# Performance work log

Measured on AMD Instinct MI355X. Metric: run time of the kernel, lower is better.

## Reference

```python
import jax, jax.numpy as jnp
import numpy as np

B, N, H, D, K, HEADS = 128, 64, 256, 128, 8, 3


def _ln(x, g, b):
    mu = x.mean(-1, keepdims=True)
    var = x.var(-1, keepdims=True)
    return (x - mu) * jax.lax.rsqrt(var + 1e-5) * g + b


def _mmlp2(x, W1, b1, g1, be1, W2, b2):
    # per-node batched MLP: [B,N,in] x [N,in,out] -> [B,N,out]
    h = jnp.einsum('bni,nio->bno', x, W1) + b1
    h = jax.nn.relu(_ln(h, g1, be1))
    return jnp.einsum('bni,nio->bno', h, W2) + b2


def _chi(x, m1, m2):
    # 2-additive Mobius Choquet integral, averaged over heads.
    # x: [B,S,K,D], m1: [S,heads,K] (singleton Mobius), m2: [S,heads,K,K] (pair Mobius, upper-tri)
    tri = jnp.triu(jnp.ones((K, K), x.dtype), k=1)
    pairmin = jnp.minimum(x[:, :, :, None, :], x[:, :, None, :, :])  # [B,S,K,K,D]
    single = jnp.einsum('shk,bskd->bsd', m1, x)
    pair = jnp.einsum('shij,bsijd->bsd', m2 * tri, pairmin)
    return (single + pair) / HEADS


def setup_inputs() -> dict:
    key = jax.random.key(0)
    ks = jax.random.split(key, 10)
    s = lambda k, *sh: (jax.random.normal(k, sh, jnp.float32) * 0.05)
    inp = {}
    inp['observation'] = jax.random.normal(ks[0], (B, N, H), jnp.float32)
    inp['action'] = jax.random.normal(ks[1], (B, N, H), jnp.float32)
    inp['local_edges'] = jax.random.randint(ks[2], (N, 2, K + 1), 0, N)
    inp['V_W1'] = s(ks[3], N, H, H);   inp['V_b1'] = jnp.zeros((N, H), jnp.float32)
    inp['V_g1'] = jnp.ones((H,), jnp.float32); inp['V_beta1'] = jnp.zeros((H,), jnp.float32)
    inp['V_W2'] = s(ks[4], N, H, D);   inp['V_b2'] = jnp.zeros((N, D), jnp.float32)
    inp['A_W1'] = s(ks[5], N, 2 * H, H); inp['A_b1'] = jnp.zeros((N, H), jnp.float32)
    inp['A_g1'] = jnp.ones((H,), jnp.float32); inp['A_beta1'] = jnp.zeros((H,), jnp.float32)
    inp['A_W2'] = s(ks[6], N, H, D);   inp['A_b2'] = jnp.zeros((N, D), jnp.float32)
    inp['chi_m1'] = s(ks[7], N, HEADS, K)
    inp['chi_m2'] = s(ks[8], N, HEADS, K, K)
    return inp


def reference(observation, action, local_edges, V_W1, V_b1, V_g1, V_beta1, V_W2, V_b2,
              A_W1, A_b1, A_g1, A_beta1, A_W2, A_b2, chi_m1, chi_m2):
    V = _mmlp2(observation, V_W1, V_b1, V_g1, V_beta1, V_W2, V_b2)          # [B,N,D]
    A = _mmlp2(jnp.concatenate([observation, action], -1),
               A_W1, A_b1, A_g1, A_beta1, A_W2, A_b2)                       # [B,N,D]
    Q = A + V
    centers = local_edges[:, 0, 0]   # [S]
    neigh = local_edges[:, 0, 1:]    # [S,K]
    # .data in torch detaches the gathered neighbors
    Qn = jax.lax.stop_gradient(Q[:, neigh, :])   # [B,S,K,D]
    Vn = jax.lax.stop_gradient(V[:, neigh, :])
    chi_q = (_chi(Qn, chi_m1, chi_m2) + Q[:, centers, :]).mean(-1)  # [B,S]
    chi_v = (_chi(Vn, chi_m1, chi_m2) + V[:, centers, :]).mean(-1)  # [B,S]
    return chi_q, chi_v
```

## Files before the change

### kernel.cpp

```cpp
#include <hip/hip_runtime.h>
#include <hip/hip_bf16.h>

#define BCNT 128
#define NNODE 64
#define HDIM 256
#define DDIM 128
#define KNEI 8
#define NR (BCNT * NNODE)

typedef __attribute__((ext_vector_type(8))) short bf16x8;
typedef __attribute__((ext_vector_type(8))) unsigned short ushort8;
typedef __attribute__((ext_vector_type(16))) float f32x16;

__device__ __forceinline__ unsigned short f2bf(float f) {
    union { __hip_bfloat16 b; unsigned short u; } c;
    c.b = __float2bfloat16(f);
    return c.u;
}
__device__ __forceinline__ float bf2f(unsigned short u) {
    union { unsigned short u; __hip_bfloat16 b; } c;
    c.u = u;
    return __bfloat162float(c.b);
}

__global__ __launch_bounds__(256) void xsplit(
    const float* __restrict__ obs, const float* __restrict__ act,
    ushort* __restrict__ obsH, ushort* __restrict__ obsL,
    ushort* __restrict__ actH, ushort* __restrict__ actL)
{
    size_t i = ((size_t)blockIdx.x * 256 + threadIdx.x) * 4;
    const size_t NT = (size_t)NR * HDIM;
    const float* src; ushort *dh, *dl;
    if (i < NT) { src = obs; dh = obsH; dl = obsL; }
    else        { i -= NT; src = act; dh = actH; dl = actL; }
    float4 v = *(const float4*)(src + i);
    ushort4 h4, l4;
    h4.x = f2bf(v.x); l4.x = f2bf(v.x - bf2f(h4.x));
    h4.y = f2bf(v.y); l4.y = f2bf(v.y - bf2f(h4.y));
    h4.z = f2bf(v.z); l4.z = f2bf(v.z - bf2f(h4.z));
    h4.w = f2bf(v.w); l4.w = f2bf(v.w - bf2f(h4.w));
    *(ushort4*)(dh + i) = h4;
    *(ushort4*)(dl + i) = l4;
}

template<int KDIM>
__global__ __launch_bounds__(128) void mlp1_mfma(
    const ushort* __restrict__ obsH, const ushort* __restrict__ obsL,
    const ushort* __restrict__ actH, const ushort* __restrict__ actL,
    const float* __restrict__ W1, const float* __restrict__ b1,
    float* __restrict__ h, float* __restrict__ statsP)
{
    const int id = blockIdx.x;
    const int s_ = (id >> 3) & 3;
    const int g_ = ((id >> 5) << 3) | (id & 7);
    const int n  = g_ >> 2;
    const int cb = g_ & 3;
    const int bm = s_ * 32;

    const int tid = threadIdx.x;
    const int l = tid & 63;
    const int wc = tid >> 6;
    const int lo32 = l & 31, gg = l >> 5;

    __shared__ __align__(16) ushort xs[2][2][32 * 40];
    __shared__ float sstat[2][32][2];

    const int oW = cb * 64 + wc * 32 + lo32;
    const float* wp = W1 + (size_t)n * KDIM * HDIM + oW;

    const int sm = tid >> 2, sc = tid & 3;
    const size_t xrow = ((size_t)(bm + sm) * NNODE + n) * HDIM;

    f32x16 acc = {};
    ushort8 xh, xl;
    float wvA_[16], wvB_[16];

    auto loadX = [&](int k0) {
        const ushort *sh = obsH, *sl = obsL;
        int kk = k0;
        if (KDIM == 512 && k0 >= 256) { sh = actH; sl = actL; kk = k0 - 256; }
        xh = *(const ushort8*)(sh + xrow + kk + sc * 8);
        xl = *(const ushort8*)(sl + xrow + kk + sc * 8);
    };

#define LOADW1(k0, wv) { _Pragma("unroll") for (int kb = 0; kb < 2; ++kb) { _Pragma("unroll") for (int i = 0; i < 8; ++i) wv[kb*8+i] = wp[(size_t)((k0) + kb*16 + gg*8 + i) * HDIM]; } }

#define STEP1(k0, buf, wvC, wvN) { \
    *(ushort8*)&xs[buf][0][sm * 40 + sc * 8] = xh; \
    *(ushort8*)&xs[buf][1][sm * 40 + sc * 8] = xl; \
    __syncthreads(); \
    if ((k0) + 32 < KDIM) { loadX((k0) + 32); LOADW1((k0) + 32, wvN); } \
    _Pragma("unroll") for (int kb = 0; kb < 2; ++kb) { \
        bf16x8 ahi = *(const bf16x8*)&xs[buf][0][lo32 * 40 + kb * 16 + gg * 8]; \
        bf16x8 alo = *(const bf16x8*)&xs[buf][1][lo32 * 40 + kb * 16 + gg * 8]; \
        bf16x8 bhi, blo; \
        _Pragma("unroll") for (int i = 0; i < 8; ++i) { \
            float f = wvC[kb*8+i]; \
            unsigned short hh = f2bf(f); \
            bhi[i] = (short)hh; \
            blo[i] = (short)f2bf(f - bf2f(hh)); \
        } \
        acc = __builtin_amdgcn_mfma_f32_32x32x16_bf16(ahi, bhi, acc, 0, 0, 0); \
        acc = __builtin_amdgcn_mfma_f32_32x32x16_bf16(ahi, blo, acc, 0, 0, 0); \
        acc = __builtin_amdgcn_mfma_f32_32x32x16_bf16(alo, bhi, acc, 0, 0, 0); \
    } \
}

    loadX(0);
    LOADW1(0, wvA_);
    #pragma unroll
    for (int k0 = 0; k0 < KDIM; k0 += 64) {
        STEP1(k0, 0, wvA_, wvB_);
        STEP1(k0 + 32, 1, wvB_, wvA_);
    }
#undef STEP1
#undef LOADW1

    float bias = b1[(size_t)n * HDIM + oW];
    #pragma unroll
    for (int r = 0; r < 16; ++r) {
        int mm = (r & 3) + 8 * (r >> 2) + 4 * gg;
        float v = acc[r] + bias;
        h[((size_t)(bm + mm) * NNODE + n) * HDIM + oW] = v;
        float a = v, q = v * v;
        #pragma unroll
        for (int off = 16; off >= 1; off >>= 1) {
            a += __shfl_xor(a, off);
            q += __shfl_xor(q, off);
        }
        if (lo32 == 0) { sstat[wc][mm][0] = a; sstat[wc][mm][1] = q; }
    }
    __syncthreads();
    if (tid < 32) {
        float s1 = sstat[0][tid][0] + sstat[1][tid][0];
        float s2 = sstat[0][tid][1] + sstat[1][tid][1];
        size_t row = (size_t)(bm + tid) * NNODE + n;
        statsP[((size_t)cb * NR + row) * 2 + 0] = s1;
        statsP[((size_t)cb * NR + row) * 2 + 1] = s2;
    }
}

__global__ __launch_bounds__(256) void lnsplit(
    const float* __restrict__ hV, const float* __restrict__ hA,
    const float* __restrict__ stV, const float* __restrict__ stA,
    const float* __restrict__ Vg1, const float* __restrict__ Vbe1,
    const float* __restrict__ Ag1, const float* __restrict__ Abe1,
    ushort* __restrict__ hbVH, ushort* __restrict__ hbVL,
    ushort* __restrict__ hbAH, ushort* __restrict__ hbAL)
{
    const int br = blockIdx.y;
    const float* hp = br ? hA : hV;
    const float* st = br ? stA : stV;
    const float* gp = br ? Ag1 : Vg1;
    const float* bp = br ? Abe1 : Vbe1;
    ushort* oh = br ? hbAH : hbVH;
    ushort* ol = br ? hbAL : hbVL;

    const int tid = threadIdx.x;
    const int row = blockIdx.x * 4 + (tid >> 6);
    const int c4 = (tid & 63) * 4;

    float s1 = 0.f, s2 = 0.f;
    #pragma unroll
    for (int cb = 0; cb < 4; ++cb) {
        s1 += st[((size_t)cb * NR + row) * 2 + 0];
        s2 += st[((size_t)cb * NR + row) * 2 + 1];
    }
    float mu = s1 * (1.0f / 256.0f);
    float rs = rsqrtf(s2 * (1.0f / 256.0f) - mu * mu + 1e-5f);

    float4 v = *(const float4*)(hp + (size_t)row * HDIM + c4);
    float4 gv = *(const float4*)(gp + c4);
    float4 bv = *(const float4*)(bp + c4);
    float y0 = fmaxf((v.x - mu) * rs * gv.x + bv.x, 0.0f);
    float y1 = fmaxf((v.y - mu) * rs * gv.y + bv.y, 0.0f);
    float y2 = fmaxf((v.z - mu) * rs * gv.z + bv.z, 0.0f);
    float y3 = fmaxf((v.w - mu) * rs * gv.w + bv.w, 0.0f);
    ushort4 h4, l4;
    h4.x = f2bf(y0); l4.x = f2bf(y0 - bf2f(h4.x));
    h4.y = f2bf(y1); l4.y = f2bf(y1 - bf2f(h4.y));
    h4.z = f2bf(y2); l4.z = f2bf(y2 - bf2f(h4.z));
    h4.w = f2bf(y3); l4.w = f2bf(y3 - bf2f(h4.w));
    *(ushort4*)(oh + (size_t)row * HDIM + c4) = h4;
    *(ushort4*)(ol + (size_t)row * HDIM + c4) = l4;
}

__global__ __launch_bounds__(128) void mlp2_mfma(
    const ushort* __restrict__ hbVH, const ushort* __restrict__ hbVL,
    const ushort* __restrict__ hbAH, const ushort* __restrict__ hbAL,
    const float* __restrict__ VW2, const float* __restrict__ Vb2,
    const float* __restrict__ AW2, const float* __restrict__ Ab2,
    float* __restrict__ Vout, float* __restrict__ Aout)
{
    const int id = blockIdx.x;
    const int s_ = (id >> 3) & 3;
    const int g_ = ((id >> 5) << 3) | (id & 7);
    const int n  = g_ >> 2;
    const int cb = g_ & 1;
    const int br = (g_ >> 1) & 1;
    const int bm = s_ * 32;

    const int tid = threadIdx.x;
    const int l = tid & 63;
    const int wc = tid >> 6;
    const int lo32 = l & 31, gg = l >> 5;

    __shared__ __align__(16) ushort xs[2][2][32 * 40];

    const int oW = cb * 64 + wc * 32 + lo32;
    const float* wp = (br ? AW2 : VW2) + (size_t)n * HDIM * DDIM + oW;
    const ushort* xph = br ? hbAH : hbVH;
    const ushort* xpl = br ? hbAL : hbVL;

    const int sm = tid >> 2, sc = tid & 3;
    const size_t xrow = ((size_t)(bm + sm) * NNODE + n) * HDIM;

    f32x16 acc = {};
    ushort8 xh, xl;
    float wvA_[16], wvB_[16];

    auto loadX = [&](int k0) {
        xh = *(const ushort8*)(xph + xrow + k0 + sc * 8);
        xl = *(const ushort8*)(xpl + xrow + k0 + sc * 8);
    };

#define LOADW2(k0, wv) { _Pragma("unroll") for (int kb = 0; kb < 2; ++kb) { _Pragma("unroll") for (int i = 0; i < 8; ++i) wv[kb*8+i] = wp[(size_t)((k0) + kb*16 + gg*8 + i) * DDIM]; } }

#define STEP2(k0, buf, wvC, wvN) { \
    *(ushort8*)&xs[buf][0][sm * 40 + sc * 8] = xh; \
    *(ushort8*)&xs[buf][1][sm * 40 + sc * 8] = xl; \
    __syncthreads(); \
    if ((k0) + 32 < HDIM) { loadX((k0) + 32); LOADW2((k0) + 32, wvN); } \
    _Pragma("unroll") for (int kb = 0; kb < 2; ++kb) { \
        bf16x8 ahi = *(const bf16x8*)&xs[buf][0][lo32 * 40 + kb * 16 + gg * 8]; \
        bf16x8 alo = *(const bf16x8*)&xs[buf][1][lo32 * 40 + kb * 16 + gg * 8]; \
        bf16x8 bhi, blo; \
        _Pragma("unroll") for (int i = 0; i < 8; ++i) { \
            float f = wvC[kb*8+i]; \
            unsigned short hh = f2bf(f); \
            bhi[i] = (short)hh; \
            blo[i] = (short)f2bf(f - bf2f(hh)); \
        } \
        acc = __builtin_amdgcn_mfma_f32_32x32x16_bf16(ahi, bhi, acc, 0, 0, 0); \
        acc = __builtin_amdgcn_mfma_f32_32x32x16_bf16(ahi, blo, acc, 0, 0, 0); \
        acc = __builtin_amdgcn_mfma_f32_32x32x16_bf16(alo, bhi, acc, 0, 0, 0); \
    } \
}

    loadX(0);
    LOADW2(0, wvA_);
    #pragma unroll
    for (int k0 = 0; k0 < HDIM; k0 += 64) {
        STEP2(k0, 0, wvA_, wvB_);
        STEP2(k0 + 32, 1, wvB_, wvA_);
    }
#undef STEP2
#undef LOADW2

    float bias = (br ? Ab2 : Vb2)[(size_t)n * DDIM + oW];
    float* outp = br ? Aout : Vout;
    #pragma unroll
    for (int r = 0; r < 16; ++r) {
        int mm = (r & 3) + 8 * (r >> 2) + 4 * gg;
        outp[((size_t)(bm + mm) * NNODE + n) * DDIM + oW] = acc[r] + bias;
    }
}

__global__ __launch_bounds__(128) void chi_kernel(
    const float* __restrict__ V, const float* __restrict__ A,
    const int* __restrict__ le, const float* __restrict__ m1,
    const float* __restrict__ m2, float* __restrict__ out)
{
    const int n = blockIdx.x;
    const int b = blockIdx.y;
    const int tid = threadIdx.x;

    __shared__ float sm1[KNEI];
    __shared__ float sm2[KNEI * KNEI];
    __shared__ int   sidx[KNEI + 1];
    __shared__ float pq[2], pv[2];

    if (tid < KNEI) {
        float s = 0.0f;
        #pragma unroll
        for (int hh = 0; hh < 3; ++hh) s += m1[n * 24 + hh * 8 + tid];
        sm1[tid] = s;
    }
    if (tid < 64) {
        int i = tid >> 3, j = tid & 7;
        float s = 0.0f;
        if (j > i) {
            #pragma unroll
            for (int hh = 0; hh < 3; ++hh) s += m2[n * 192 + hh * 64 + tid];
        }
        sm2[tid] = s;
    }
    if (tid < KNEI + 1) sidx[tid] = le[n * 18 + tid];
    __syncthreads();

    const float* Vb_ = V + (size_t)b * (NNODE * DDIM);
    const float* Ab_ = A + (size_t)b * (NNODE * DDIM);
    const int cen = sidx[0];

    float vn[KNEI], qn[KNEI];
    #pragma unroll
    for (int k = 0; k < KNEI; ++k) {
        int nb = sidx[1 + k];
        float vv = Vb_[nb * DDIM + tid];
        float aa = Ab_[nb * DDIM + tid];
        vn[k] = vv;
        qn[k] = vv + aa;
    }

    float sq = 0.0f, sv = 0.0f;
    #pragma unroll
    for (int k = 0; k < KNEI; ++k) { sq += sm1[k] * qn[k]; sv += sm1[k] * vn[k]; }
    #pragma unroll
    for (int i = 0; i < KNEI; ++i) {
        #pragma unroll
        for (int j = i + 1; j < KNEI; ++j) {
            float w = sm2[i * 8 + j];
            sq += w * fminf(qn[i], qn[j]);
            sv += w * fminf(vn[i], vn[j]);
        }
    }

    float Vc = Vb_[cen * DDIM + tid];
    float Ac = Ab_[cen * DDIM + tid];
    float valq = sq * (1.0f / 3.0f) + (Vc + Ac);
    float valv = sv * (1.0f / 3.0f) + Vc;

    #pragma unroll
    for (int o = 32; o; o >>= 1) {
        valq += __shfl_down(valq, o);
        valv += __shfl_down(valv, o);
    }
    if ((tid & 63) == 0) { pq[tid >> 6] = valq; pv[tid >> 6] = valv; }
    __syncthreads();
    if (tid == 0) {
        out[b * NNODE + n]                = (pq[0] + pq[1]) * (1.0f / 128.0f);
        out[BCNT * NNODE + b * NNODE + n] = (pv[0] + pv[1]) * (1.0f / 128.0f);
    }
}

extern "C" void kernel_launch(void* const* d_in, const int* in_sizes, int n_in,
                              void* d_out, int out_size, void* d_ws, size_t ws_size,
                              hipStream_t stream)
{
    const float* obs  = (const float*)d_in[0];
    const float* act  = (const float*)d_in[1];
    const int*   le   = (const int*)  d_in[2];
    const float* VW1  = (const float*)d_in[3];
    const float* Vb1  = (const float*)d_in[4];
    const float* Vg1  = (const float*)d_in[5];
    const float* Vbe1 = (const float*)d_in[6];
    const float* VW2  = (const float*)d_in[7];
    const float* Vb2  = (const float*)d_in[8];
    const float* AW1  = (const float*)d_in[9];
    const float* Ab1  = (const float*)d_in[10];
    const float* Ag1  = (const float*)d_in[11];
    const float* Abe1 = (const float*)d_in[12];
    const float* AW2  = (const float*)d_in[13];
    const float* Ab2  = (const float*)d_in[14];
    const float* m1   = (const float*)d_in[15];
    const float* m2   = (const float*)d_in[16];
    float* out = (float*)d_out;

    float* hV  = (float*)d_ws;
    float* hA  = hV + (size_t)NR * HDIM;
    float* V   = hA + (size_t)NR * HDIM;
    float* A   = V  + (size_t)NR * DDIM;
    float* stV = A  + (size_t)NR * DDIM;
    float* stA = stV + (size_t)4 * NR * 2;
    ushort* up = (ushort*)(stA + (size_t)4 * NR * 2);
    const size_t P = (size_t)NR * HDIM;
    ushort* obsH = up;          ushort* obsL = obsH + P;
    ushort* actH = obsL + P;    ushort* actL = actH + P;
    ushort* hbVH = actL + P;    ushort* hbVL = hbVH + P;
    ushort* hbAH = hbVL + P;    ushort* hbAL = hbAH + P;

    xsplit<<<dim3(4096), dim3(256), 0, stream>>>(obs, act, obsH, obsL, actH, actL);
    mlp1_mfma<256><<<dim3(1024), dim3(128), 0, stream>>>(obsH, obsL, actH, actL,
                                                         VW1, Vb1, hV, stV);
    mlp1_mfma<512><<<dim3(1024), dim3(128), 0, stream>>>(obsH, obsL, actH, actL,
                                                         AW1, Ab1, hA, stA);
    lnsplit<<<dim3(NR / 4, 2), dim3(256), 0, stream>>>(hV, hA, stV, stA,
                                                       Vg1, Vbe1, Ag1, Abe1,
                                                       hbVH, hbVL, hbAH, hbAL);
    mlp2_mfma<<<dim3(1024), dim3(128), 0, stream>>>(hbVH, hbVL, hbAH, hbAL,
                                                    VW2, Vb2, AW2, Ab2, V, A);
    chi_kernel<<<dim3(NNODE, BCNT), dim3(128), 0, stream>>>(V, A, le, m1, m2, out);
}
```

Before: 203.1 us.

## Pre-split and transpose weights, fuse MLP layer-1 with LayerNorm epilogue

Adds a wsplit kernel that transposes all four weight tensors and splits them once into bf16 hi/lo planes. The MFMA kernels can then load B fragments as contiguous 16-byte vectors instead of strided scalar fp32 loads with per-element conversion. The V and A layer-1 GEMMs merge into one 256-thread kernel where each block covers the full 256-wide hidden row. That lets LayerNorm statistics, ReLU and the hi/lo split run in the epilogue, which removes the fp32 hidden buffer, the partial-stats buffer and the separate lnsplit pass. In exchange the weights are re-split on every call, adding one extra pass over them, and mlp1 now runs fewer, larger blocks that hold more registers.

```diff
diff --git a/kernel.cpp b/kernel.cpp
--- a/kernel.cpp
+++ b/kernel.cpp
@@ -8,6 +8,12 @@
 #define KNEI 8
 #define NR (BCNT * NNODE)
 
+#define OFF1V 0
+#define OFF1A 4194304
+#define OFF2V 12582912
+#define OFF2A 14680064
+#define WTOT  16777216
+
 typedef __attribute__((ext_vector_type(8))) short bf16x8;
 typedef __attribute__((ext_vector_type(8))) unsigned short ushort8;
 typedef __attribute__((ext_vector_type(16))) float f32x16;
@@ -21,6 +27,50 @@
     union { unsigned short u; __hip_bfloat16 b; } c;
     c.u = u;
     return __bfloat162float(c.b);
+}
+__device__ __forceinline__ void split2(float f, unsigned short& h, unsigned short& l) {
+    h = f2bf(f);
+    l = f2bf(f - bf2f(h));
+}
+
+__global__ __launch_bounds__(256) void wsplit(
+    const float* __restrict__ VW1, const float* __restrict__ AW1,
+    const float* __restrict__ VW2, const float* __restrict__ AW2,
+    ushort* __restrict__ WtH, ushort* __restrict__ WtL)
+{
+    const int n = blockIdx.y;
+    const int t = blockIdx.x;
+    const float* src; size_t dbase; int K, OUT, tk, to;
+    if (t < 16)      { src = VW1 + (size_t)n*65536;  dbase = OFF1V + (size_t)n*65536;  K=256; OUT=256; tk=t>>2;      to=t&3;      }
+    else if (t < 48) { src = AW1 + (size_t)n*131072; dbase = OFF1A + (size_t)n*131072; K=512; OUT=256; tk=(t-16)>>2; to=(t-16)&3; }
+    else if (t < 56) { src = VW2 + (size_t)n*32768;  dbase = OFF2V + (size_t)n*32768;  K=256; OUT=128; tk=(t-48)>>1; to=(t-48)&1; }
+    else             { src = AW2 + (size_t)n*32768;  dbase = OFF2A + (size_t)n*32768;  K=256; OUT=128; tk=(t-56)>>1; to=(t-56)&1; }
+    const int k0 = tk*64, o0 = to*64;
+    __shared__ float tile[64][65];
+    const int tid = threadIdx.x;
+    const int rr = tid>>2, cc = (tid&3)*16;
+    #pragma unroll
+    for (int j=0;j<4;++j){
+        float4 v = *(const float4*)(src + (size_t)(k0+rr)*OUT + (o0+cc+j*4));
+        tile[rr][cc+j*4+0]=v.x; tile[rr][cc+j*4+1]=v.y;
+        tile[rr][cc+j*4+2]=v.z; tile[rr][cc+j*4+3]=v.w;
+    }
+    __syncthreads();
+    const int orow = tid>>2, kc = (tid&3)*16;
+    ushort8 h8a, h8b, l8a, l8b;
+    #pragma unroll
+    for (int j=0;j<8;++j){
+        unsigned short hh, ll;
+        split2(tile[kc+j][orow], hh, ll);
+        h8a[j]=hh; l8a[j]=ll;
+        split2(tile[kc+8+j][orow], hh, ll);
+        h8b[j]=hh; l8b[j]=ll;
+    }
+    size_t d = dbase + (size_t)(o0+orow)*K + (k0+kc);
+    *(ushort8*)(WtH + d)     = h8a;
+    *(ushort8*)(WtH + d + 8) = h8b;
+    *(ushort8*)(WtL + d)     = l8a;
+    *(ushort8*)(WtL + d + 8) = l8b;
 }
 
 __global__ __launch_bounds__(256) void xsplit(
@@ -35,234 +85,219 @@
     else        { i -= NT; src = act; dh = actH; dl = actL; }
     float4 v = *(const float4*)(src + i);
     ushort4 h4, l4;
-    h4.x = f2bf(v.x); l4.x = f2bf(v.x - bf2f(h4.x));
-    h4.y = f2bf(v.y); l4.y = f2bf(v.y - bf2f(h4.y));
-    h4.z = f2bf(v.z); l4.z = f2bf(v.z - bf2f(h4.z));
-    h4.w = f2bf(v.w); l4.w = f2bf(v.w - bf2f(h4.w));
+    split2(v.x, h4.x, l4.x);
+    split2(v.y, h4.y, l4.y);
+    split2(v.z, h4.z, l4.z);
+    split2(v.w, h4.w, l4.w);
     *(ushort4*)(dh + i) = h4;
     *(ushort4*)(dl + i) = l4;
 }
 
-template<int KDIM>
-__global__ __launch_bounds__(128) void mlp1_mfma(
+__global__ __launch_bounds__(256) void mlp1_fused(
     const ushort* __restrict__ obsH, const ushort* __restrict__ obsL,
     const ushort* __restrict__ actH, const ushort* __restrict__ actL,
-    const float* __restrict__ W1, const float* __restrict__ b1,
-    float* __restrict__ h, float* __restrict__ statsP)
-{
-    const int id = blockIdx.x;
-    const int s_ = (id >> 3) & 3;
-    const int g_ = ((id >> 5) << 3) | (id & 7);
-    const int n  = g_ >> 2;
-    const int cb = g_ & 3;
-    const int bm = s_ * 32;
-
-    const int tid = threadIdx.x;
-    const int l = tid & 63;
-    const int wc = tid >> 6;
-    const int lo32 = l & 31, gg = l >> 5;
-
-    __shared__ __align__(16) ushort xs[2][2][32 * 40];
-    __shared__ float sstat[2][32][2];
-
-    const int oW = cb * 64 + wc * 32 + lo32;
-    const float* wp = W1 + (size_t)n * KDIM * HDIM + oW;
-
-    const int sm = tid >> 2, sc = tid & 3;
-    const size_t xrow = ((size_t)(bm + sm) * NNODE + n) * HDIM;
-
-    f32x16 acc = {};
-    ushort8 xh, xl;
-    float wvA_[16], wvB_[16];
-
-    auto loadX = [&](int k0) {
-        const ushort *sh = obsH, *sl = obsL;
-        int kk = k0;
-        if (KDIM == 512 && k0 >= 256) { sh = actH; sl = actL; kk = k0 - 256; }
-        xh = *(const ushort8*)(sh + xrow + kk + sc * 8);
-        xl = *(const ushort8*)(sl + xrow + kk + sc * 8);
-    };
-
-#define LOADW1(k0, wv) { _Pragma("unroll") for (int kb = 0; kb < 2; ++kb) { _Pragma("unroll") for (int i = 0; i < 8; ++i) wv[kb*8+i] = wp[(size_t)((k0) + kb*16 + gg*8 + i) * HDIM]; } }
-
-#define STEP1(k0, buf, wvC, wvN) { \
-    *(ushort8*)&xs[buf][0][sm * 40 + sc * 8] = xh; \
-    *(ushort8*)&xs[buf][1][sm * 40 + sc * 8] = xl; \
-    __syncthreads(); \
-    if ((k0) + 32 < KDIM) { loadX((k0) + 32); LOADW1((k0) + 32, wvN); } \
-    _Pragma("unroll") for (int kb = 0; kb < 2; ++kb) { \
-        bf16x8 ahi = *(const bf16x8*)&xs[buf][0][lo32 * 40 + kb * 16 + gg * 8]; \
-        bf16x8 alo = *(const bf16x8*)&xs[buf][1][lo32 * 40 + kb * 16 + gg * 8]; \
-        bf16x8 bhi, blo; \
-        _Pragma("unroll") for (int i = 0; i < 8; ++i) { \
-            float f = wvC[kb*8+i]; \
-            unsigned short hh = f2bf(f); \
-            bhi[i] = (short)hh; \
-            blo[i] = (short)f2bf(f - bf2f(hh)); \
-        } \
-        acc = __builtin_amdgcn_mfma_f32_32x32x16_bf16(ahi, bhi, acc, 0, 0, 0); \
-        acc = __builtin_amdgcn_mfma_f32_32x32x16_bf16(ahi, blo, acc, 0, 0, 0); \
-        acc = __builtin_amdgcn_mfma_f32_32x32x16_bf16(alo, bhi, acc, 0, 0, 0); \
-    } \
-}
-
-    loadX(0);
-    LOADW1(0, wvA_);
-    #pragma unroll
-    for (int k0 = 0; k0 < KDIM; k0 += 64) {
-        STEP1(k0, 0, wvA_, wvB_);
-        STEP1(k0 + 32, 1, wvB_, wvA_);
-    }
-#undef STEP1
-#undef LOADW1
-
-    float bias = b1[(size_t)n * HDIM + oW];
-    #pragma unroll
-    for (int r = 0; r < 16; ++r) {
-        int mm = (r & 3) + 8 * (r >> 2) + 4 * gg;
-        float v = acc[r] + bias;
-        h[((size_t)(bm + mm) * NNODE + n) * HDIM + oW] = v;
-        float a = v, q = v * v;
-        #pragma unroll
-        for (int off = 16; off >= 1; off >>= 1) {
-            a += __shfl_xor(a, off);
-            q += __shfl_xor(q, off);
-        }
-        if (lo32 == 0) { sstat[wc][mm][0] = a; sstat[wc][mm][1] = q; }
-    }
-    __syncthreads();
-    if (tid < 32) {
-        float s1 = sstat[0][tid][0] + sstat[1][tid][0];
-        float s2 = sstat[0][tid][1] + sstat[1][tid][1];
-        size_t row = (size_t)(bm + tid) * NNODE + n;
-        statsP[((size_t)cb * NR + row) * 2 + 0] = s1;
-        statsP[((size_t)cb * NR + row) * 2 + 1] = s2;
-    }
-}
-
-__global__ __launch_bounds__(256) void lnsplit(
-    const float* __restrict__ hV, const float* __restrict__ hA,
-    const float* __restrict__ stV, const float* __restrict__ stA,
+    const ushort* __restrict__ WtH, const ushort* __restrict__ WtL,
+    const float* __restrict__ Vb1, const float* __restrict__ Ab1,
     const float* __restrict__ Vg1, const float* __restrict__ Vbe1,
     const float* __restrict__ Ag1, const float* __restrict__ Abe1,
     ushort* __restrict__ hbVH, ushort* __restrict__ hbVL,
     ushort* __restrict__ hbAH, ushort* __restrict__ hbAL)
 {
-    const int br = blockIdx.y;
-    const float* hp = br ? hA : hV;
-    const float* st = br ? stA : stV;
-    const float* gp = br ? Ag1 : Vg1;
-    const float* bp = br ? Abe1 : Vbe1;
-    ushort* oh = br ? hbAH : hbVH;
-    ushort* ol = br ? hbAL : hbVL;
+    const int id = blockIdx.x;
+    const int s_ = (id>>3)&3;
+    const int g_ = ((id>>5)<<3)|(id&7);
+    const int n  = g_>>1;
+    const int br = g_&1;
+    const int bm = s_*32;
+    const int KD = br ? 512 : 256;
 
     const int tid = threadIdx.x;
-    const int row = blockIdx.x * 4 + (tid >> 6);
-    const int c4 = (tid & 63) * 4;
-
-    float s1 = 0.f, s2 = 0.f;
-    #pragma unroll
-    for (int cb = 0; cb < 4; ++cb) {
-        s1 += st[((size_t)cb * NR + row) * 2 + 0];
-        s2 += st[((size_t)cb * NR + row) * 2 + 1];
-    }
-    float mu = s1 * (1.0f / 256.0f);
-    float rs = rsqrtf(s2 * (1.0f / 256.0f) - mu * mu + 1e-5f);
-
-    float4 v = *(const float4*)(hp + (size_t)row * HDIM + c4);
-    float4 gv = *(const float4*)(gp + c4);
-    float4 bv = *(const float4*)(bp + c4);
-    float y0 = fmaxf((v.x - mu) * rs * gv.x + bv.x, 0.0f);
-    float y1 = fmaxf((v.y - mu) * rs * gv.y + bv.y, 0.0f);
-    float y2 = fmaxf((v.z - mu) * rs * gv.z + bv.z, 0.0f);
-    float y3 = fmaxf((v.w - mu) * rs * gv.w + bv.w, 0.0f);
-    ushort4 h4, l4;
-    h4.x = f2bf(y0); l4.x = f2bf(y0 - bf2f(h4.x));
-    h4.y = f2bf(y1); l4.y = f2bf(y1 - bf2f(h4.y));
-    h4.z = f2bf(y2); l4.z = f2bf(y2 - bf2f(h4.z));
-    h4.w = f2bf(y3); l4.w = f2bf(y3 - bf2f(h4.w));
-    *(ushort4*)(oh + (size_t)row * HDIM + c4) = h4;
-    *(ushort4*)(ol + (size_t)row * HDIM + c4) = l4;
+    const int l = tid&63, w_ = tid>>6;
+    const int lo32 = l&31, gg = l>>5;
+
+    __shared__ ushort8 xs[2][256];
+    __shared__ float2 wsum[8][16];
+    __shared__ float2 lnp[32];
+
+    const size_t wtoff = br ? (size_t)OFF1A + (size_t)n*131072
+                            : (size_t)OFF1V + (size_t)n*65536;
+    const size_t wcol0 = wtoff + (size_t)(w_*64 + lo32)*KD;
+    const size_t wcol1 = wtoff + (size_t)(w_*64 + 32 + lo32)*KD;
+
+    const int srow = tid&31, sc = (tid>>5)&3, sp = tid>>7;
+    const size_t xgrow = ((size_t)(bm+srow)*NNODE + n)*HDIM;
+
+    f32x16 acc0 = {}; f32x16 acc1 = {};
+    ushort8 xcur, xnxt;
+    bf16x8 bh0[2], bh1[2], bl0[2], bl1[2];
+    bf16x8 nh0[2], nh1[2], nl0[2], nl1[2];
+
+    auto loadX = [&](int k0, ushort8& x){
+        const ushort* plane;
+        int kk = k0 & 255;
+        if (br && k0 >= 256) plane = sp ? actL : actH;
+        else                 plane = sp ? obsL : obsH;
+        x = *(const ushort8*)(plane + xgrow + kk + sc*8);
+    };
+    auto loadB = [&](int k0, bf16x8* h0, bf16x8* h1, bf16x8* l0, bf16x8* l1){
+        #pragma unroll
+        for (int kb=0;kb<2;++kb){
+            size_t o0 = wcol0 + k0 + kb*16 + gg*8;
+            size_t o1 = wcol1 + k0 + kb*16 + gg*8;
+            h0[kb] = *(const bf16x8*)(WtH + o0);
+            l0[kb] = *(const bf16x8*)(WtL + o0);
+            h1[kb] = *(const bf16x8*)(WtH + o1);
+            l1[kb] = *(const bf16x8*)(WtL + o1);
+        }
+    };
+
+#define MSTEP(K0, BUF, BH0, BH1, BL0, BL1, NH0, NH1, NL0, NL1, XC, XN) { \
+    xs[BUF][(sp*4+sc)*32 + srow] = XC; \
+    __syncthreads(); \
+    if ((K0)+32 < KD) { loadX((K0)+32, XN); loadB((K0)+32, NH0, NH1, NL0, NL1); } \
+    _Pragma("unroll") \
+    for (int kb=0;kb<2;++kb){ \
+        bf16x8 ah = *(const bf16x8*)&xs[BUF][(kb*2+gg)*32 + lo32]; \
+        bf16x8 al = *(const bf16x8*)&xs[BUF][(4 + kb*2+gg)*32 + lo32]; \
+        acc0 = __builtin_amdgcn_mfma_f32_32x32x16_bf16(ah, BH0[kb], acc0, 0,0,0); \
+        acc0 = __builtin_amdgcn_mfma_f32_32x32x16_bf16(ah, BL0[kb], acc0, 0,0,0); \
+        acc0 = __builtin_amdgcn_mfma_f32_32x32x16_bf16(al, BH0[kb], acc0, 0,0,0); \
+        acc1 = __builtin_amdgcn_mfma_f32_32x32x16_bf16(ah, BH1[kb], acc1, 0,0,0); \
+        acc1 = __builtin_amdgcn_mfma_f32_32x32x16_bf16(ah, BL1[kb], acc1, 0,0,0); \
+        acc1 = __builtin_amdgcn_mfma_f32_32x32x16_bf16(al, BH1[kb], acc1, 0,0,0); \
+    } }
+
+    loadX(0, xcur);
+    loadB(0, bh0, bh1, bl0, bl1);
+    for (int k0 = 0; k0 < KD; k0 += 64) {
+        MSTEP(k0,    0, bh0,bh1,bl0,bl1, nh0,nh1,nl0,nl1, xcur, xnxt);
+        MSTEP(k0+32, 1, nh0,nh1,nl0,nl1, bh0,bh1,bl0,bl1, xnxt, xcur);
+    }
+#undef MSTEP
+
+    const float* b1p = (br ? Ab1 : Vb1) + (size_t)n*HDIM;
+    const float* gp  = br ? Ag1 : Vg1;
+    const float* bep = br ? Abe1 : Vbe1;
+    const float bias0 = b1p[w_*64 + lo32];
+    const float bias1 = b1p[w_*64 + 32 + lo32];
+    float v0[16], v1[16], s[16], q[16];
+    #pragma unroll
+    for (int r=0;r<16;++r){
+        v0[r]=acc0[r]+bias0; v1[r]=acc1[r]+bias1;
+        s[r]=v0[r]+v1[r]; q[r]=v0[r]*v0[r]+v1[r]*v1[r];
+    }
+    #pragma unroll
+    for (int off=1; off<32; off<<=1){
+        #pragma unroll
+        for (int r=0;r<16;++r){ s[r]+=__shfl_xor(s[r],off); q[r]+=__shfl_xor(q[r],off); }
+    }
+    if (lo32==0){
+        #pragma unroll
+        for (int r=0;r<16;++r) wsum[w_*2+gg][r] = float2{s[r], q[r]};
+    }
+    __syncthreads();
+    if (tid < 32){
+        const int row=tid, ggr=(row>>2)&1, r=(row&3)|((row>>3)<<2);
+        float ss=0.f, qq=0.f;
+        #pragma unroll
+        for (int w=0;w<4;++w){ float2 p=wsum[w*2+ggr][r]; ss+=p.x; qq+=p.y; }
+        float mu = ss*(1.0f/256.0f);
+        float var = qq*(1.0f/256.0f) - mu*mu;
+        lnp[row] = float2{mu, rsqrtf(var + 1e-5f)};
+    }
+    __syncthreads();
+    ushort* oH = br ? hbAH : hbVH;
+    ushort* oL = br ? hbAL : hbVL;
+    const float g0 = gp[w_*64+lo32],    be0 = bep[w_*64+lo32];
+    const float g1 = gp[w_*64+32+lo32], be1 = bep[w_*64+32+lo32];
+    #pragma unroll
+    for (int r=0;r<16;++r){
+        const int mm = (r&3)+8*(r>>2)+4*gg;
+        float2 p = lnp[mm];
+        size_t base = ((size_t)(bm+mm)*NNODE + n)*HDIM + w_*64;
+        float y0 = fmaxf((v0[r]-p.x)*p.y*g0 + be0, 0.0f);
+        float y1 = fmaxf((v1[r]-p.x)*p.y*g1 + be1, 0.0f);
+        unsigned short hh, ll;
+        split2(y0, hh, ll); oH[base+lo32]=hh;    oL[base+lo32]=ll;
+        split2(y1, hh, ll); oH[base+32+lo32]=hh; oL[base+32+lo32]=ll;
+    }
 }
 
 __global__ __launch_bounds__(128) void mlp2_mfma(
     const ushort* __restrict__ hbVH, const ushort* __restrict__ hbVL,
     const ushort* __restrict__ hbAH, const ushort* __restrict__ hbAL,
-    const float* __restrict__ VW2, const float* __restrict__ Vb2,
-    const float* __restrict__ AW2, const float* __restrict__ Ab2,
+    const ushort* __restrict__ WtH, const ushort* __restrict__ WtL,
+    const float* __restrict__ Vb2, const float* __restrict__ Ab2,
     float* __restrict__ Vout, float* __restrict__ Aout)
 {
     const int id = blockIdx.x;
-    const int s_ = (id >> 3) & 3;
-    const int g_ = ((id >> 5) << 3) | (id & 7);
-    const int n  = g_ >> 2;
-    const int cb = g_ & 1;
-    const int br = (g_ >> 1) & 1;
-    const int bm = s_ * 32;
+    const int s_ = (id>>3)&3;
+    const int g_ = ((id>>5)<<3)|(id&7);
+    const int n  = g_>>2;
+    const int cb = g_&1;
+    const int br = (g_>>1)&1;
+    const int bm = s_*32;
 
     const int tid = threadIdx.x;
-    const int l = tid & 63;
-    const int wc = tid >> 6;
-    const int lo32 = l & 31, gg = l >> 5;
-
-    __shared__ __align__(16) ushort xs[2][2][32 * 40];
-
-    const int oW = cb * 64 + wc * 32 + lo32;
-    const float* wp = (br ? AW2 : VW2) + (size_t)n * HDIM * DDIM + oW;
-    const ushort* xph = br ? hbAH : hbVH;
-    const ushort* xpl = br ? hbAL : hbVL;
-
-    const int sm = tid >> 2, sc = tid & 3;
-    const size_t xrow = ((size_t)(bm + sm) * NNODE + n) * HDIM;
+    const int l = tid&63, wc = tid>>6;
+    const int lo32=l&31, gg=l>>5;
+
+    __shared__ ushort8 xs[2][256];
+
+    const size_t wtoff = (br ? (size_t)OFF2A : (size_t)OFF2V) + (size_t)n*32768;
+    const int oW = cb*64 + wc*32 + lo32;
+    const size_t wcol = wtoff + (size_t)oW*HDIM;
+
+    const ushort* xH = br ? hbAH : hbVH;
+    const ushort* xL = br ? hbAL : hbVL;
+    const int srow = tid&31, sc = tid>>5;
+    const size_t xgrow = ((size_t)(bm+srow)*NNODE + n)*HDIM;
 
     f32x16 acc = {};
-    ushort8 xh, xl;
-    float wvA_[16], wvB_[16];
-
-    auto loadX = [&](int k0) {
-        xh = *(const ushort8*)(xph + xrow + k0 + sc * 8);
-        xl = *(const ushort8*)(xpl + xrow + k0 + sc * 8);
+    ushort8 xhc, xlc, xhn, xln;
+    bf16x8 bh[2], bl[2], nh[2], nl[2];
+
+    auto loadX2 = [&](int k0, ushort8& xh, ushort8& xl){
+        xh = *(const ushort8*)(xH + xgrow + k0 + sc*8);
+        xl = *(const ushort8*)(xL + xgrow + k0 + sc*8);
     };
-
-#define LOADW2(k0, wv) { _Pragma("unroll") for (int kb = 0; kb < 2; ++kb) { _Pragma("unroll") for (int i = 0; i < 8; ++i) wv[kb*8+i] = wp[(size_t)((k0) + kb*16 + gg*8 + i) * DDIM]; } }
-
-#define STEP2(k0, buf, wvC, wvN) { \
-    *(ushort8*)&xs[buf][0][sm * 40 + sc * 8] = xh; \
-    *(ushort8*)&xs[buf][1][sm * 40 + sc * 8] = xl; \
+    auto loadB2 = [&](int k0, bf16x8* h, bf16x8* lo){
+        #pragma unroll
+        for (int kb=0;kb<2;++kb){
+            size_t o = wcol + k0 + kb*16 + gg*8;
+            h[kb]  = *(const bf16x8*)(WtH + o);
+            lo[kb] = *(const bf16x8*)(WtL + o);
+        }
+    };
+
+#define MSTEP2(K0, BUF, BH, BL, NH, NL, XHC, XLC, XHN, XLN) { \
+    xs[BUF][sc*32 + srow] = XHC; \
+    xs[BUF][(4+sc)*32 + srow] = XLC; \
     __syncthreads(); \
-    if ((k0) + 32 < HDIM) { loadX((k0) + 32); LOADW2((k0) + 32, wvN); } \
-    _Pragma("unroll") for (int kb = 0; kb < 2; ++kb) { \
-        bf16x8 ahi = *(const bf16x8*)&xs[buf][0][lo32 * 40 + kb * 16 + gg * 8]; \
-        bf16x8 alo = *(const bf16x8*)&xs[buf][1][lo32 * 40 + kb * 16 + gg * 8]; \
-        bf16x8 bhi, blo; \
-        _Pragma("unroll") for (int i = 0; i < 8; ++i) { \
-            float f = wvC[kb*8+i]; \
-            unsigned short hh = f2bf(f); \
-            bhi[i] = (short)hh; \
-            blo[i] = (short)f2bf(f - bf2f(hh)); \
-        } \
-        acc = __builtin_amdgcn_mfma_f32_32x32x16_bf16(ahi, bhi, acc, 0, 0, 0); \
-        acc = __builtin_amdgcn_mfma_f32_32x32x16_bf16(ahi, blo, acc, 0, 0, 0); \
-        acc = __builtin_amdgcn_mfma_f32_32x32x16_bf16(alo, bhi, acc, 0, 0, 0); \
-    } \
-}
-
-    loadX(0);
-    LOADW2(0, wvA_);
-    #pragma unroll
+    if ((K0)+32 < HDIM) { loadX2((K0)+32, XHN, XLN); loadB2((K0)+32, NH, NL); } \
+    _Pragma("unroll") \
+    for (int kb=0;kb<2;++kb){ \
+        bf16x8 ah = *(const bf16x8*)&xs[BUF][(kb*2+gg)*32 + lo32]; \
+        bf16x8 al = *(const bf16x8*)&xs[BUF][(4 + kb*2+gg)*32 + lo32]; \
+        acc = __builtin_amdgcn_mfma_f32_32x32x16_bf16(ah, BH[kb], acc, 0,0,0); \
+        acc = __builtin_amdgcn_mfma_f32_32x32x16_bf16(ah, BL[kb], acc, 0,0,0); \
+        acc = __builtin_amdgcn_mfma_f32_32x32x16_bf16(al, BH[kb], acc, 0,0,0); \
+    } }
+
+    loadX2(0, xhc, xlc);
+    loadB2(0, bh, bl);
     for (int k0 = 0; k0 < HDIM; k0 += 64) {
-        STEP2(k0, 0, wvA_, wvB_);
-        STEP2(k0 + 32, 1, wvB_, wvA_);
-    }
-#undef STEP2
-#undef LOADW2
-
-    float bias = (br ? Ab2 : Vb2)[(size_t)n * DDIM + oW];
+        MSTEP2(k0,    0, bh,bl, nh,nl, xhc,xlc, xhn,xln);
+        MSTEP2(k0+32, 1, nh,nl, bh,bl, xhn,xln, xhc,xlc);
+    }
+#undef MSTEP2
+
+    const float bias = (br ? Ab2 : Vb2)[(size_t)n*DDIM + oW];
     float* outp = br ? Aout : Vout;
     #pragma unroll
-    for (int r = 0; r < 16; ++r) {
-        int mm = (r & 3) + 8 * (r >> 2) + 4 * gg;
-        outp[((size_t)(bm + mm) * NNODE + n) * DDIM + oW] = acc[r] + bias;
+    for (int r=0;r<16;++r){
+        const int mm = (r&3)+8*(r>>2)+4*gg;
+        outp[((size_t)(bm+mm)*NNODE + n)*DDIM + oW] = acc[r] + bias;
     }
 }
 
@@ -366,28 +401,26 @@
     const float* m2   = (const float*)d_in[16];
     float* out = (float*)d_out;
 
-    float* hV  = (float*)d_ws;
-    float* hA  = hV + (size_t)NR * HDIM;
-    float* V   = hA + (size_t)NR * HDIM;
-    float* A   = V  + (size_t)NR * DDIM;
-    float* stV = A  + (size_t)NR * DDIM;
-    float* stA = stV + (size_t)4 * NR * 2;
-    ushort* up = (ushort*)(stA + (size_t)4 * NR * 2);
     const size_t P = (size_t)NR * HDIM;
-    ushort* obsH = up;          ushort* obsL = obsH + P;
-    ushort* actH = obsL + P;    ushort* actL = actH + P;
-    ushort* hbVH = actL + P;    ushort* hbVL = hbVH + P;
-    ushort* hbAH = hbVL + P;    ushort* hbAL = hbAH + P;
-
+    ushort* WtH  = (ushort*)d_ws;
+    ushort* WtL  = WtH + WTOT;
+    ushort* obsH = WtL + WTOT;
+    ushort* obsL = obsH + P;
+    ushort* actH = obsL + P;
+    ushort* actL = actH + P;
+    ushort* hbVH = actL + P;
+    ushort* hbVL = hbVH + P;
+    ushort* hbAH = hbVL + P;
+    ushort* hbAL = hbAH + P;
+    float*  V    = (float*)(hbAL + P);
+    float*  A    = V + (size_t)NR * DDIM;
+
+    wsplit<<<dim3(64, 64), dim3(256), 0, stream>>>(VW1, AW1, VW2, AW2, WtH, WtL);
     xsplit<<<dim3(4096), dim3(256), 0, stream>>>(obs, act, obsH, obsL, actH, actL);
-    mlp1_mfma<256><<<dim3(1024), dim3(128), 0, stream>>>(obsH, obsL, actH, actL,
-                                                         VW1, Vb1, hV, stV);
-    mlp1_mfma<512><<<dim3(1024), dim3(128), 0, stream>>>(obsH, obsL, actH, actL,
-                                                         AW1, Ab1, hA, stA);
-    lnsplit<<<dim3(NR / 4, 2), dim3(256), 0, stream>>>(hV, hA, stV, stA,
-                                                       Vg1, Vbe1, Ag1, Abe1,
-                                                       hbVH, hbVL, hbAH, hbAL);
-    mlp2_mfma<<<dim3(1024), dim3(128), 0, stream>>>(hbVH, hbVL, hbAH, hbAL,
-                                                    VW2, Vb2, AW2, Ab2, V, A);
+    mlp1_fused<<<dim3(512), dim3(256), 0, stream>>>(obsH, obsL, actH, actL, WtH, WtL,
+                                                    Vb1, Ab1, Vg1, Vbe1, Ag1, Abe1,
+                                                    hbVH, hbVL, hbAH, hbAL);
+    mlp2_mfma<<<dim3(1024), dim3(128), 0, stream>>>(hbVH, hbVL, hbAH, hbAL, WtH, WtL,
+                                                    Vb2, Ab2, V, A);
     chi_kernel<<<dim3(NNODE, BCNT), dim3(128), 0, stream>>>(V, A, le, m1, m2, out);
 }
```

Result: slower. 232.1 us (+14.2%).
